# Kernel optimization log

Hardware: AMD Instinct MI355X
Metric: run time of the kernel (lower is better)

Reference implementation:

```python
import jax, jax.numpy as jnp
import numpy as np

N, K, F_IN, T, OUT = 50000, 25, 128, 256, 128
EPS = 1e-3  # TF BatchNormalization default epsilon


def batchnorm_train(x, gamma, beta):
    # training-mode BN: biased batch statistics over axis 0
    mean = jnp.mean(x, axis=0)
    var = jnp.var(x, axis=0)
    return (x - mean) * jax.lax.rsqrt(var + EPS) * gamma + beta


def setup_inputs() -> dict:
    key = jax.random.key(0)
    ks = jax.random.split(key, 6)
    return {
        "self_nodes": jax.random.normal(ks[0], (N, F_IN), dtype=jnp.float32),
        "neigh_nodes": jax.random.normal(ks[1], (N, K, F_IN), dtype=jnp.float32),
        "len_adj_nodes": jax.random.randint(ks[2], (N,), 1, K + 1, dtype=jnp.int32),
        "Wt": jax.random.normal(ks[3], (F_IN, T), dtype=jnp.float32) * 0.05,
        "bt": jnp.zeros((T,), dtype=jnp.float32),
        "g1": jnp.ones((T,), dtype=jnp.float32),
        "b1": jnp.zeros((T,), dtype=jnp.float32),
        "Wn": jax.random.normal(ks[4], (T, OUT), dtype=jnp.float32) * 0.05,
        "Ws": jax.random.normal(ks[5], (F_IN, OUT), dtype=jnp.float32) * 0.05,
        "g2": jnp.ones((2 * OUT,), dtype=jnp.float32),
        "b2": jnp.zeros((2 * OUT,), dtype=jnp.float32),
    }


def reference(self_nodes, neigh_nodes, len_adj_nodes, Wt, bt, g1, b1, Wn, Ws, g2, b2):
    # len_adj_nodes is accepted by the original call() but unused.
    # transform neighbor features: [N, K, F_IN] -> [N, K, T]
    neigh = jnp.einsum('nkf,ft->nkt', neigh_nodes, Wt) + bt
    # bn1 over flattened [N*K, T] (training mode)
    neigh = batchnorm_train(neigh.reshape(-1, T), g1, b1).reshape(N, K, T)
    # pool_op = reduce_max over the neighbor axis
    pooled = jnp.max(neigh, axis=1)            # [N, T]
    neigh_out = pooled @ Wn                     # [N, OUT], no bias
    self_out = self_nodes @ Ws                  # [N, OUT], no bias
    out = jnp.concatenate([self_out, neigh_out], axis=1)  # use_concat=True
    out = batchnorm_train(out, g2, b2)
    return jax.nn.relu(out)
```

## Files before the change

### kernel.cpp

```cpp
#include <hip/hip_runtime.h>


#define NN 50000
#define KN 25
#define FIN 128
#define TD 256
#define OUTD 128
#define BN_EPS 1e-3f
#define NSLOTS 64
#define K1_GRID 512
#define NGROUPS (NN / 2)

typedef float f32x4 __attribute__((ext_vector_type(4)));
typedef short bf16x8 __attribute__((ext_vector_type(8)));

__device__ __forceinline__ ushort f2bf(float f) {
    uint u = __builtin_bit_cast(uint, f);
    return (ushort)((u + 0x7FFFu + ((u >> 16) & 1u)) >> 16);
}
__device__ __forceinline__ uint pk2(float a, float b) {
    return (uint)f2bf(a) | ((uint)f2bf(b) << 16);
}

__global__ __launch_bounds__(256, 2) void k1_gemm_pool(
    const float* __restrict__ neigh, const float* __restrict__ Wt,
    const float* __restrict__ bt, float* __restrict__ nmax,
    float* __restrict__ nmin, float* __restrict__ s1sum, float* __restrict__ s1sq)
{
    __shared__ ushort lds[32768];
    const int tid = threadIdx.x;
    const int wave = tid >> 6, lane = tid & 63;
    const int quad = lane >> 4, l16 = lane & 15;
    const int cbase = wave * 64;

    {
        const float4* w4 = (const float4*)Wt;
        #pragma unroll
        for (int i = 0; i < 32; ++i) {
            const int e = tid + i * 256;
            const int k = e >> 6, c4 = (e & 63) << 2;
            const float4 v = w4[e];
            uint* dst = (uint*)&lds[k * 256 + c4];
            dst[0] = pk2(v.x, v.y);
            dst[1] = pk2(v.z, v.w);
        }
    }
    __syncthreads();

    bf16x8 bf[4][4];
    #pragma unroll
    for (int nt = 0; nt < 4; ++nt) {
        const int col = cbase + nt * 16 + l16;
        #pragma unroll
        for (int ks = 0; ks < 4; ++ks) {
            #pragma unroll
            for (int j = 0; j < 8; ++j)
                bf[nt][ks][j] = (short)lds[(ks * 32 + quad * 8 + j) * 256 + col];
        }
    }
    __syncthreads();

    float bv[4];
    #pragma unroll
    for (int n = 0; n < 4; ++n) bv[n] = bt[cbase + n * 16 + l16];

    float S[4] = {0.f, 0.f, 0.f, 0.f}, Q[4] = {0.f, 0.f, 0.f, 0.f};

    int g = blockIdx.x;
    {
        const float2* src = (const float2*)(neigh + (size_t)g * 6400);
        #pragma unroll
        for (int i = 0; i < 13; ++i) {
            const int idx = tid + i * 256;
            if (idx < 3200) {
                const float2 v = src[idx];
                const int r = idx >> 6;
                const int pr = r + (r >= 25 ? 7 : 0);
                *(uint*)&lds[pr * 136 + ((idx & 63) << 1)] = pk2(v.x, v.y);
            }
        }
    }
    __syncthreads();

    int cur = 0;
    for (; g < NGROUPS; g += K1_GRID) {
        const int gn = g + K1_GRID;
        float2 pre[13];
        if (gn < NGROUPS) {
            const float2* src = (const float2*)(neigh + (size_t)gn * 6400);
            #pragma unroll
            for (int i = 0; i < 13; ++i) {
                const int idx = tid + i * 256;
                if (idx < 3200) pre[i] = src[idx];
            }
        }
        const ushort* Ab = lds + cur * 8704;
        f32x4 acc[4][4];
        #pragma unroll
        for (int m = 0; m < 4; ++m)
            #pragma unroll
            for (int n = 0; n < 4; ++n)
                acc[m][n] = (f32x4){0.f, 0.f, 0.f, 0.f};
        #pragma unroll
        for (int m = 0; m < 4; ++m) {
            bf16x8 af[4];
            #pragma unroll
            for (int ks = 0; ks < 4; ++ks)
                af[ks] = *(const bf16x8*)&Ab[(m * 16 + l16) * 136 + ks * 32 + quad * 8];
            #pragma unroll
            for (int n = 0; n < 4; ++n)
                #pragma unroll
                for (int ks = 0; ks < 4; ++ks)
                    acc[m][n] = __builtin_amdgcn_mfma_f32_16x16x32_bf16(af[ks], bf[n][ks], acc[m][n], 0, 0, 0);
        }
        #pragma unroll
        for (int gi = 0; gi < 2; ++gi) {
            const int node = g * 2 + gi;
            #pragma unroll
            for (int n = 0; n < 4; ++n) {
                float mx = -3.4e38f, mn = 3.4e38f;
                #pragma unroll
                for (int i = 0; i < 4; ++i) {
                    const float v = acc[2 * gi][n][i] + bv[n];
                    mx = fmaxf(mx, v); mn = fminf(mn, v);
                    S[n] += v; Q[n] = fmaf(v, v, Q[n]);
                }
                #pragma unroll
                for (int i = 0; i < 4; ++i) {
                    if (quad * 4 + i < 9) {
                        const float v = acc[2 * gi + 1][n][i] + bv[n];
                        mx = fmaxf(mx, v); mn = fminf(mn, v);
                        S[n] += v; Q[n] = fmaf(v, v, Q[n]);
                    }
                }
                mx = fmaxf(mx, __shfl_xor(mx, 16)); mx = fmaxf(mx, __shfl_xor(mx, 32));
                mn = fminf(mn, __shfl_xor(mn, 16)); mn = fminf(mn, __shfl_xor(mn, 32));
                if (lane < 16) {
                    const int o = node * TD + cbase + n * 16 + lane;
                    nmax[o] = mx; nmin[o] = mn;
                }
            }
        }
        if (gn < NGROUPS) {
            ushort* Aw = lds + (cur ^ 1) * 8704;
            #pragma unroll
            for (int i = 0; i < 13; ++i) {
                const int idx = tid + i * 256;
                if (idx < 3200) {
                    const int r = idx >> 6;
                    const int pr = r + (r >= 25 ? 7 : 0);
                    *(uint*)&Aw[pr * 136 + ((idx & 63) << 1)] = pk2(pre[i].x, pre[i].y);
                }
            }
        }
        __syncthreads();
        cur ^= 1;
    }
    #pragma unroll
    for (int n = 0; n < 4; ++n) {
        float s = S[n]; s += __shfl_xor(s, 16); s += __shfl_xor(s, 32);
        float q = Q[n]; q += __shfl_xor(q, 16); q += __shfl_xor(q, 32);
        if (lane < 16) {
            const int col = cbase + n * 16 + lane;
            const int slot = blockIdx.x & (NSLOTS - 1);
            atomicAdd(&s1sum[slot * TD + col], s);
            atomicAdd(&s1sq[slot * TD + col], q);
        }
    }
}

__global__ __launch_bounds__(256) void k_stats(
    const float* __restrict__ ssum, const float* __restrict__ ssq,
    const float* __restrict__ g, const float* __restrict__ b,
    float invM, float* __restrict__ a, float* __restrict__ cc)
{
    const int c = threadIdx.x;
    float s = 0.f, q = 0.f;
    for (int j = 0; j < NSLOTS; ++j) { s += ssum[j * TD + c]; q += ssq[j * TD + c]; }
    const float mean = s * invM;
    const float var = q * invM - mean * mean;
    const float A = rsqrtf(var + BN_EPS) * g[c];
    a[c] = A;
    cc[c] = fmaf(-mean, A, b[c]);
}

__global__ __launch_bounds__(256, 2) void k2_gemm2(
    const float* __restrict__ selfn, const float* __restrict__ nmax,
    const float* __restrict__ nmin, const float* __restrict__ Ws,
    const float* __restrict__ Wn, const float* __restrict__ a1,
    const float* __restrict__ c1, float* __restrict__ Y,
    float* __restrict__ s2sum, float* __restrict__ s2sq)
{
    __shared__ ushort lds[25600];
    const int tid = threadIdx.x;
    const int wave = tid >> 6, lane = tid & 63;
    const int quad = lane >> 4, l16 = lane & 15;
    const int R0 = blockIdx.x * 64;

    {
        const float4* s4 = (const float4*)selfn;
        #pragma unroll
        for (int i = 0; i < 8; ++i) {
            const int e = tid + i * 256;
            const int r = e >> 5, k4 = e & 31;
            const int gr = R0 + r;
            const float4 v = (gr < NN) ? s4[(size_t)gr * 32 + k4] : make_float4(0.f, 0.f, 0.f, 0.f);
            uint* dst = (uint*)&lds[r * 136 + (k4 << 2)];
            dst[0] = pk2(v.x, v.y);
            dst[1] = pk2(v.z, v.w);
        }
    }
    {
        const float4* mx4 = (const float4*)nmax;
        const float4* mn4 = (const float4*)nmin;
        const float4* a4p = (const float4*)a1;
        const float4* c4p = (const float4*)c1;
        #pragma unroll
        for (int i = 0; i < 16; ++i) {
            const int e = tid + i * 256;
            const int r = e >> 6, c4 = e & 63;
            const int gr = R0 + r;
            const float4 vx = (gr < NN) ? mx4[(size_t)gr * 64 + c4] : make_float4(0.f, 0.f, 0.f, 0.f);
            const float4 vn = (gr < NN) ? mn4[(size_t)gr * 64 + c4] : make_float4(0.f, 0.f, 0.f, 0.f);
            const float4 a = a4p[c4], c = c4p[c4];
            const float p0 = (a.x >= 0.f) ? fmaf(a.x, vx.x, c.x) : fmaf(a.x, vn.x, c.x);
            const float p1 = (a.y >= 0.f) ? fmaf(a.y, vx.y, c.y) : fmaf(a.y, vn.y, c.y);
            const float p2 = (a.z >= 0.f) ? fmaf(a.z, vx.z, c.z) : fmaf(a.z, vn.z, c.z);
            const float p3 = (a.w >= 0.f) ? fmaf(a.w, vx.w, c.w) : fmaf(a.w, vn.w, c.w);
            uint* dst = (uint*)&lds[8704 + r * 264 + (c4 << 2)];
            dst[0] = pk2(p0, p1);
            dst[1] = pk2(p2, p3);
        }
    }
    __syncthreads();

    f32x4 acc[4][4];
    #pragma unroll
    for (int m = 0; m < 4; ++m)
        #pragma unroll
        for (int n = 0; n < 4; ++n)
            acc[m][n] = (f32x4){0.f, 0.f, 0.f, 0.f};

    if (wave < 2) {
        const int cb = wave * 64;
        bf16x8 bfr[4][4];
        #pragma unroll
        for (int nt = 0; nt < 4; ++nt)
            #pragma unroll
            for (int ks = 0; ks < 4; ++ks)
                #pragma unroll
                for (int j = 0; j < 8; ++j)
                    bfr[nt][ks][j] = (short)f2bf(Ws[(ks * 32 + quad * 8 + j) * OUTD + cb + nt * 16 + l16]);
        #pragma unroll
        for (int m = 0; m < 4; ++m) {
            bf16x8 af[4];
            #pragma unroll
            for (int ks = 0; ks < 4; ++ks)
                af[ks] = *(const bf16x8*)&lds[(m * 16 + l16) * 136 + ks * 32 + quad * 8];
            #pragma unroll
            for (int nt = 0; nt < 4; ++nt)
                #pragma unroll
                for (int ks = 0; ks < 4; ++ks)
                    acc[m][nt] = __builtin_amdgcn_mfma_f32_16x16x32_bf16(af[ks], bfr[nt][ks], acc[m][nt], 0, 0, 0);
        }
    } else {
        const int cb = (wave - 2) * 64;
        bf16x8 bfr[4][8];
        #pragma unroll
        for (int nt = 0; nt < 4; ++nt)
            #pragma unroll
            for (int ks = 0; ks < 8; ++ks)
                #pragma unroll
                for (int j = 0; j < 8; ++j)
                    bfr[nt][ks][j] = (short)f2bf(Wn[(ks * 32 + quad * 8 + j) * OUTD + cb + nt * 16 + l16]);
        #pragma unroll
        for (int m = 0; m < 4; ++m) {
            bf16x8 af[8];
            #pragma unroll
            for (int ks = 0; ks < 8; ++ks)
                af[ks] = *(const bf16x8*)&lds[8704 + (m * 16 + l16) * 264 + ks * 32 + quad * 8];
            #pragma unroll
            for (int nt = 0; nt < 4; ++nt)
                #pragma unroll
                for (int ks = 0; ks < 8; ++ks)
                    acc[m][nt] = __builtin_amdgcn_mfma_f32_16x16x32_bf16(af[ks], bfr[nt][ks], acc[m][nt], 0, 0, 0);
        }
    }

    const int colb = wave * 64;
    float S[4] = {0.f, 0.f, 0.f, 0.f}, Q[4] = {0.f, 0.f, 0.f, 0.f};
    #pragma unroll
    for (int m = 0; m < 4; ++m) {
        #pragma unroll
        for (int nt = 0; nt < 4; ++nt) {
            #pragma unroll
            for (int i = 0; i < 4; ++i) {
                const int row = R0 + m * 16 + quad * 4 + i;
                const float v = acc[m][nt][i];
                if (row < NN) {
                    Y[(size_t)row * TD + colb + nt * 16 + l16] = v;
                    S[nt] += v;
                    Q[nt] = fmaf(v, v, Q[nt]);
                }
            }
        }
    }
    #pragma unroll
    for (int nt = 0; nt < 4; ++nt) {
        float s = S[nt]; s += __shfl_xor(s, 16); s += __shfl_xor(s, 32);
        float q = Q[nt]; q += __shfl_xor(q, 16); q += __shfl_xor(q, 32);
        if (lane < 16) {
            const int col = colb + nt * 16 + lane;
            const int slot = blockIdx.x & (NSLOTS - 1);
            atomicAdd(&s2sum[slot * TD + col], s);
            atomicAdd(&s2sq[slot * TD + col], q);
        }
    }
}

__global__ __launch_bounds__(256) void k7_bn_relu(
    float* __restrict__ out, const float* __restrict__ a2, const float* __restrict__ c2)
{
    const int idx = blockIdx.x * 256 + threadIdx.x;
    const int c4 = idx & 63;
    float4 y = ((const float4*)out)[idx];
    const float4 a = ((const float4*)a2)[c4];
    const float4 c = ((const float4*)c2)[c4];
    y.x = fmaxf(0.f, fmaf(a.x, y.x, c.x));
    y.y = fmaxf(0.f, fmaf(a.y, y.y, c.y));
    y.z = fmaxf(0.f, fmaf(a.z, y.z, c.z));
    y.w = fmaxf(0.f, fmaf(a.w, y.w, c.w));
    ((float4*)out)[idx] = y;
}

extern "C" void kernel_launch(void* const* d_in, const int* in_sizes, int n_in,
                              void* d_out, int out_size, void* d_ws, size_t ws_size,
                              hipStream_t stream) {
    const float* selfn = (const float*)d_in[0];
    const float* neigh = (const float*)d_in[1];
    const float* Wt = (const float*)d_in[3];
    const float* bt = (const float*)d_in[4];
    const float* g1 = (const float*)d_in[5];
    const float* b1 = (const float*)d_in[6];
    const float* Wn = (const float*)d_in[7];
    const float* Ws = (const float*)d_in[8];
    const float* g2 = (const float*)d_in[9];
    const float* b2 = (const float*)d_in[10];
    float* out = (float*)d_out;

    float* ws = (float*)d_ws;
    float* nmax = ws;
    float* nmin = nmax + (size_t)NN * TD;
    float* s1sum = nmin + (size_t)NN * TD;
    float* s1sq = s1sum + NSLOTS * TD;
    float* s2sum = s1sq + NSLOTS * TD;
    float* s2sq = s2sum + NSLOTS * TD;
    float* a1 = s2sq + NSLOTS * TD;
    float* c1 = a1 + TD;
    float* a2 = c1 + TD;
    float* c2 = a2 + TD;

    hipMemsetAsync(s1sum, 0, (size_t)4 * NSLOTS * TD * sizeof(float), stream);

    k1_gemm_pool<<<K1_GRID, 256, 0, stream>>>(neigh, Wt, bt, nmax, nmin, s1sum, s1sq);
    k_stats<<<1, 256, 0, stream>>>(s1sum, s1sq, g1, b1, 1.f / (float)(NN * KN), a1, c1);
    k2_gemm2<<<(NN + 63) / 64, 256, 0, stream>>>(selfn, nmax, nmin, Ws, Wn, a1, c1, out, s2sum, s2sq);
    k_stats<<<1, 256, 0, stream>>>(s2sum, s2sq, g2, b2, 1.f / (float)NN, a2, c2);
    k7_bn_relu<<<NN * TD / 4 / 256, 256, 0, stream>>>(out, a2, c2);
}
```

Baseline: 996.8 us.

## Pack pooled max/min as bf16, pretranspose weights, fold BN1 stats into GEMM2

Pooled max and min now go out as one packed bf16 pair per element instead of two fp32 arrays, which halves the intermediate write and read traffic between the two GEMM kernels. A new prep kernel zeroes the stats buffers and pre-transposes Ws/Wn to bf16, replacing the memset and the per-block scalar weight gathers in k2. The BN1 statistics reduction moves into k2's prologue, removing one launch, and k1 reads its neighbor tiles with float4 loads. The cost is that every k2 block re-reduces the 64 stat slots, and max/min are rounded to bf16 before normalization.

```diff
diff --git a/kernel.cpp b/kernel.cpp
--- a/kernel.cpp
+++ b/kernel.cpp
@@ -21,11 +21,33 @@
 __device__ __forceinline__ uint pk2(float a, float b) {
     return (uint)f2bf(a) | ((uint)f2bf(b) << 16);
 }
+__device__ __forceinline__ float bflo(uint u) {
+    return __builtin_bit_cast(float, u << 16);
+}
+__device__ __forceinline__ float bfhi(uint u) {
+    return __builtin_bit_cast(float, u & 0xffff0000u);
+}
+
+__global__ __launch_bounds__(256) void k0_prep(
+    const float* __restrict__ Ws, const float* __restrict__ Wn,
+    float* __restrict__ stats, ushort* __restrict__ WsT, ushort* __restrict__ WnT)
+{
+    const int gid = blockIdx.x * 256 + threadIdx.x;
+    if (gid < 65536) {
+        stats[gid] = 0.f;
+    } else if (gid < 81920) {
+        const int t = gid - 65536, col = t >> 7, k = t & 127;
+        WsT[col * FIN + k] = f2bf(Ws[k * OUTD + col]);
+    } else {
+        const int t = gid - 81920, col = t >> 8, k = t & 255;
+        WnT[col * TD + k] = f2bf(Wn[k * OUTD + col]);
+    }
+}
 
 __global__ __launch_bounds__(256, 2) void k1_gemm_pool(
     const float* __restrict__ neigh, const float* __restrict__ Wt,
-    const float* __restrict__ bt, float* __restrict__ nmax,
-    float* __restrict__ nmin, float* __restrict__ s1sum, float* __restrict__ s1sq)
+    const float* __restrict__ bt, uint* __restrict__ nmm,
+    float* __restrict__ s1sum, float* __restrict__ s1sq)
 {
     __shared__ ushort lds[32768];
     const int tid = threadIdx.x;
@@ -68,15 +90,17 @@
 
     int g = blockIdx.x;
     {
-        const float2* src = (const float2*)(neigh + (size_t)g * 6400);
-        #pragma unroll
-        for (int i = 0; i < 13; ++i) {
+        const float4* src = (const float4*)(neigh + (size_t)g * 6400);
+        #pragma unroll
+        for (int i = 0; i < 7; ++i) {
             const int idx = tid + i * 256;
-            if (idx < 3200) {
-                const float2 v = src[idx];
-                const int r = idx >> 6;
+            if (idx < 1600) {
+                const float4 v = src[idx];
+                const int r = idx >> 5;
                 const int pr = r + (r >= 25 ? 7 : 0);
-                *(uint*)&lds[pr * 136 + ((idx & 63) << 1)] = pk2(v.x, v.y);
+                uint* dst = (uint*)&lds[pr * 136 + ((idx & 31) << 2)];
+                dst[0] = pk2(v.x, v.y);
+                dst[1] = pk2(v.z, v.w);
             }
         }
     }
@@ -85,13 +109,13 @@
     int cur = 0;
     for (; g < NGROUPS; g += K1_GRID) {
         const int gn = g + K1_GRID;
-        float2 pre[13];
+        float4 pre[7];
         if (gn < NGROUPS) {
-            const float2* src = (const float2*)(neigh + (size_t)gn * 6400);
-            #pragma unroll
-            for (int i = 0; i < 13; ++i) {
+            const float4* src = (const float4*)(neigh + (size_t)gn * 6400);
+            #pragma unroll
+            for (int i = 0; i < 7; ++i) {
                 const int idx = tid + i * 256;
-                if (idx < 3200) pre[i] = src[idx];
+                if (idx < 1600) pre[i] = src[idx];
             }
         }
         const ushort* Ab = lds + cur * 8704;
@@ -135,21 +159,21 @@
                 }
                 mx = fmaxf(mx, __shfl_xor(mx, 16)); mx = fmaxf(mx, __shfl_xor(mx, 32));
                 mn = fminf(mn, __shfl_xor(mn, 16)); mn = fminf(mn, __shfl_xor(mn, 32));
-                if (lane < 16) {
-                    const int o = node * TD + cbase + n * 16 + lane;
-                    nmax[o] = mx; nmin[o] = mn;
-                }
+                if (lane < 16)
+                    nmm[node * TD + cbase + n * 16 + lane] = pk2(mx, mn);
             }
         }
         if (gn < NGROUPS) {
             ushort* Aw = lds + (cur ^ 1) * 8704;
             #pragma unroll
-            for (int i = 0; i < 13; ++i) {
+            for (int i = 0; i < 7; ++i) {
                 const int idx = tid + i * 256;
-                if (idx < 3200) {
-                    const int r = idx >> 6;
+                if (idx < 1600) {
+                    const int r = idx >> 5;
                     const int pr = r + (r >= 25 ? 7 : 0);
-                    *(uint*)&Aw[pr * 136 + ((idx & 63) << 1)] = pk2(pre[i].x, pre[i].y);
+                    uint* dst = (uint*)&Aw[pr * 136 + ((idx & 31) << 2)];
+                    dst[0] = pk2(pre[i].x, pre[i].y);
+                    dst[1] = pk2(pre[i].z, pre[i].w);
                 }
             }
         }
@@ -185,17 +209,31 @@
 }
 
 __global__ __launch_bounds__(256, 2) void k2_gemm2(
-    const float* __restrict__ selfn, const float* __restrict__ nmax,
-    const float* __restrict__ nmin, const float* __restrict__ Ws,
-    const float* __restrict__ Wn, const float* __restrict__ a1,
-    const float* __restrict__ c1, float* __restrict__ Y,
-    float* __restrict__ s2sum, float* __restrict__ s2sq)
+    const float* __restrict__ selfn, const uint* __restrict__ nmm,
+    const ushort* __restrict__ WsT, const ushort* __restrict__ WnT,
+    const float* __restrict__ s1sum, const float* __restrict__ s1sq,
+    const float* __restrict__ g1, const float* __restrict__ b1,
+    float* __restrict__ Y, float* __restrict__ s2sum, float* __restrict__ s2sq)
 {
     __shared__ ushort lds[25600];
+    __shared__ float aL[256], cL[256];
     const int tid = threadIdx.x;
     const int wave = tid >> 6, lane = tid & 63;
     const int quad = lane >> 4, l16 = lane & 15;
     const int R0 = blockIdx.x * 64;
+
+    {
+        const int c = tid;
+        float s = 0.f, q = 0.f;
+        #pragma unroll 8
+        for (int j = 0; j < NSLOTS; ++j) { s += s1sum[j * TD + c]; q += s1sq[j * TD + c]; }
+        const float invM = 1.f / (float)((size_t)NN * KN);
+        const float mean = s * invM;
+        const float var = q * invM - mean * mean;
+        const float A = rsqrtf(var + BN_EPS) * g1[c];
+        aL[c] = A;
+        cL[c] = fmaf(-mean, A, b1[c]);
+    }
 
     {
         const float4* s4 = (const float4*)selfn;
@@ -210,23 +248,24 @@
             dst[1] = pk2(v.z, v.w);
         }
     }
+    __syncthreads();
+
     {
-        const float4* mx4 = (const float4*)nmax;
-        const float4* mn4 = (const float4*)nmin;
-        const float4* a4p = (const float4*)a1;
-        const float4* c4p = (const float4*)c1;
+        const uint4* m4 = (const uint4*)nmm;
         #pragma unroll
         for (int i = 0; i < 16; ++i) {
             const int e = tid + i * 256;
             const int r = e >> 6, c4 = e & 63;
             const int gr = R0 + r;
-            const float4 vx = (gr < NN) ? mx4[(size_t)gr * 64 + c4] : make_float4(0.f, 0.f, 0.f, 0.f);
-            const float4 vn = (gr < NN) ? mn4[(size_t)gr * 64 + c4] : make_float4(0.f, 0.f, 0.f, 0.f);
-            const float4 a = a4p[c4], c = c4p[c4];
-            const float p0 = (a.x >= 0.f) ? fmaf(a.x, vx.x, c.x) : fmaf(a.x, vn.x, c.x);
-            const float p1 = (a.y >= 0.f) ? fmaf(a.y, vx.y, c.y) : fmaf(a.y, vn.y, c.y);
-            const float p2 = (a.z >= 0.f) ? fmaf(a.z, vx.z, c.z) : fmaf(a.z, vn.z, c.z);
-            const float p3 = (a.w >= 0.f) ? fmaf(a.w, vx.w, c.w) : fmaf(a.w, vn.w, c.w);
+            uint4 v;
+            if (gr < NN) v = m4[(size_t)gr * 64 + c4];
+            else { v.x = 0u; v.y = 0u; v.z = 0u; v.w = 0u; }
+            const float4 a = *(const float4*)&aL[c4 << 2];
+            const float4 c = *(const float4*)&cL[c4 << 2];
+            const float p0 = (a.x >= 0.f) ? fmaf(a.x, bflo(v.x), c.x) : fmaf(a.x, bfhi(v.x), c.x);
+            const float p1 = (a.y >= 0.f) ? fmaf(a.y, bflo(v.y), c.y) : fmaf(a.y, bfhi(v.y), c.y);
+            const float p2 = (a.z >= 0.f) ? fmaf(a.z, bflo(v.z), c.z) : fmaf(a.z, bfhi(v.z), c.z);
+            const float p3 = (a.w >= 0.f) ? fmaf(a.w, bflo(v.w), c.w) : fmaf(a.w, bfhi(v.w), c.w);
             uint* dst = (uint*)&lds[8704 + r * 264 + (c4 << 2)];
             dst[0] = pk2(p0, p1);
             dst[1] = pk2(p2, p3);
@@ -248,9 +287,7 @@
         for (int nt = 0; nt < 4; ++nt)
             #pragma unroll
             for (int ks = 0; ks < 4; ++ks)
-                #pragma unroll
-                for (int j = 0; j < 8; ++j)
-                    bfr[nt][ks][j] = (short)f2bf(Ws[(ks * 32 + quad * 8 + j) * OUTD + cb + nt * 16 + l16]);
+                bfr[nt][ks] = *(const bf16x8*)&WsT[(cb + nt * 16 + l16) * FIN + ks * 32 + quad * 8];
         #pragma unroll
         for (int m = 0; m < 4; ++m) {
             bf16x8 af[4];
@@ -270,9 +307,7 @@
         for (int nt = 0; nt < 4; ++nt)
             #pragma unroll
             for (int ks = 0; ks < 8; ++ks)
-                #pragma unroll
-                for (int j = 0; j < 8; ++j)
-                    bfr[nt][ks][j] = (short)f2bf(Wn[(ks * 32 + quad * 8 + j) * OUTD + cb + nt * 16 + l16]);
+                bfr[nt][ks] = *(const bf16x8*)&WnT[(cb + nt * 16 + l16) * TD + ks * 32 + quad * 8];
         #pragma unroll
         for (int m = 0; m < 4; ++m) {
             bf16x8 af[8];
@@ -349,22 +384,20 @@
     float* out = (float*)d_out;
 
     float* ws = (float*)d_ws;
-    float* nmax = ws;
-    float* nmin = nmax + (size_t)NN * TD;
-    float* s1sum = nmin + (size_t)NN * TD;
+    uint* nmm = (uint*)ws;
+    float* s1sum = ws + (size_t)NN * TD;
     float* s1sq = s1sum + NSLOTS * TD;
     float* s2sum = s1sq + NSLOTS * TD;
     float* s2sq = s2sum + NSLOTS * TD;
-    float* a1 = s2sq + NSLOTS * TD;
-    float* c1 = a1 + TD;
-    float* a2 = c1 + TD;
+    float* a2 = s2sq + NSLOTS * TD;
     float* c2 = a2 + TD;
-
-    hipMemsetAsync(s1sum, 0, (size_t)4 * NSLOTS * TD * sizeof(float), stream);
-
-    k1_gemm_pool<<<K1_GRID, 256, 0, stream>>>(neigh, Wt, bt, nmax, nmin, s1sum, s1sq);
-    k_stats<<<1, 256, 0, stream>>>(s1sum, s1sq, g1, b1, 1.f / (float)(NN * KN), a1, c1);
-    k2_gemm2<<<(NN + 63) / 64, 256, 0, stream>>>(selfn, nmax, nmin, Ws, Wn, a1, c1, out, s2sum, s2sq);
+    ushort* WsT = (ushort*)(c2 + TD);
+    ushort* WnT = WsT + FIN * OUTD;
+
+    k0_prep<<<448, 256, 0, stream>>>(Ws, Wn, s1sum, WsT, WnT);
+    k1_gemm_pool<<<K1_GRID, 256, 0, stream>>>(neigh, Wt, bt, nmm, s1sum, s1sq);
+    k2_gemm2<<<(NN + 63) / 64, 256, 0, stream>>>(selfn, nmm, WsT, WnT, s1sum, s1sq,
+                                                 g1, b1, out, s2sum, s2sq);
     k_stats<<<1, 256, 0, stream>>>(s2sum, s2sq, g2, b2, 1.f / (float)NN, a2, c2);
     k7_bn_relu<<<NN * TD / 4 / 256, 256, 0, stream>>>(out, a2, c2);
 }
```

New measurement: 1.049 ms. 1.05x slower.
